# Kernel optimization log

Hardware: AMD Instinct MI355X
Metric: run time of the kernel (lower is better)

The kernel has to match this reference:

```python
import jax, jax.numpy as jnp
import numpy as np

B, S, D = 16, 2048, 128


def setup_inputs() -> dict:
    key = jax.random.key(0)
    k1, k2, k3, k4 = jax.random.split(key, 4)
    return {
        "query": jax.random.normal(k1, (B, S, D), dtype=jnp.float32),
        "key": jax.random.normal(k2, (B, S, D), dtype=jnp.float32),
        "value": jax.random.normal(k3, (B, S, D), dtype=jnp.float32),
        "scale_factor": jax.random.normal(k4, (1, S, S), dtype=jnp.float32),
        "dropout_p": 0,
    }


def reference(query, key, value, scale_factor, dropout_p):
    # qk = Q K^T  -> [B, S, S]
    qk = jnp.einsum("bqd,bkd->bqk", query, key)
    # elementwise scale matrix (broadcast over batch), then row softmax
    scaled_qk = qk * scale_factor
    softmax_qk = jax.nn.softmax(scaled_qk, axis=-1)
    # dropout_p == 0 -> identity (eval-mode / deterministic baseline)
    # output = P V -> [B, S, D]
    return jnp.einsum("bqk,bkd->bqd", softmax_qk, value)
```

## Files before the change

### kernel.cpp

```cpp
#include <hip/hip_runtime.h>
#include <hip/hip_bf16.h>

#define SS 2048
#define DD 128
#define KT 64
#define NT (SS / KT)

typedef float floatx4 __attribute__((ext_vector_type(4)));
typedef __bf16 bf16x8 __attribute__((ext_vector_type(8)));
typedef unsigned short u16x4 __attribute__((ext_vector_type(4)));
typedef unsigned short u16x8 __attribute__((ext_vector_type(8)));

__device__ __forceinline__ int kcol_perm(int d) {
    return ((d >> 5) << 5) | (((d & 15) >> 2) << 3) | (((d >> 4) & 1) << 2) | (d & 3);
}

__device__ __forceinline__ unsigned short bfbits(float x) {
    __bf16 h = (__bf16)x;
    return __builtin_bit_cast(unsigned short, h);
}

__global__ __launch_bounds__(256, 2)
void attn_scaled_kernel(const float* __restrict__ Q, const float* __restrict__ K,
                        const float* __restrict__ V, const float* __restrict__ Sc,
                        float* __restrict__ Out) {
    __shared__ __align__(16) unsigned short Khi[KT * DD];
    __shared__ __align__(16) unsigned short Klo[KT * DD];
    __shared__ __align__(16) unsigned short Vt[DD * KT];

    const int t    = threadIdx.x;
    const int w    = t >> 6;
    const int lane = t & 63;
    const int lq   = lane & 15;
    const int qg   = lane >> 4;

    const int p     = blockIdx.x;
    const int wid   = ((p & 7) << 6) + (p >> 3);
    const int batch = wid >> 5;
    const int q0    = (wid & 31) << 6;

    const float* Qb = Q + (size_t)batch * SS * DD;
    const float* Kb = K + (size_t)batch * SS * DD;
    const float* Vb = V + (size_t)batch * SS * DD;

    const int srow = t >> 5;
    const int c4   = (t & 31) << 2;
    const int kw0  = srow * 128 + (kcol_perm(c4) ^ ((srow & 7) << 3));
    const float* Kp = Kb + (size_t)srow * DD + c4;

    const int vd   = ((w & 1) << 6) + lane;
    const int vkv  = w >> 1;
    const int vswz = (vd & 7) << 3;
    const float* Vp = Vb + vd;

#define STAGE_K(I, KV) do {                                           \
        float ks_[4] = {(KV).x, (KV).y, (KV).z, (KV).w};              \
        u16x4 hh_, ll_;                                               \
        _Pragma("unroll")                                             \
        for (int e_ = 0; e_ < 4; ++e_) {                              \
            __bf16 hb_ = (__bf16)ks_[e_];                             \
            __bf16 lb_ = (__bf16)(ks_[e_] - (float)hb_);              \
            hh_[e_] = __builtin_bit_cast(unsigned short, hb_);        \
            ll_[e_] = __builtin_bit_cast(unsigned short, lb_);        \
        }                                                             \
        *(u16x4*)&Khi[kw0 + 1024 * (I)] = hh_;                        \
        *(u16x4*)&Klo[kw0 + 1024 * (I)] = ll_;                        \
    } while (0)

#define STAGE_V(I, VPI) do {                                          \
        u16x8 vv_;                                                    \
        _Pragma("unroll")                                             \
        for (int e_ = 0; e_ < 8; ++e_) vv_[e_] = bfbits((VPI)[e_]);   \
        *(u16x8*)&Vt[((vd << 6) + (vkv << 5) + ((I) << 3)) ^ vswz] = vv_; \
    } while (0)

#define LOAD_V(I, VPI, BASE) do {                                     \
        _Pragma("unroll")                                             \
        for (int h_ = 0; h_ < 2; ++h_)                                \
            _Pragma("unroll")                                         \
            for (int j_ = 0; j_ < 4; ++j_)                            \
                (VPI)[h_ * 4 + j_] =                                  \
                    Vp[(BASE) + (size_t)((vkv << 5) + ((I) << 2) + (h_ << 4) + j_) * DD]; \
    } while (0)

    const int qrow = q0 + (w << 4) + lq;
    const float* Qr = Qb + (size_t)qrow * DD;
    bf16x8 qh[4], ql[4];
#pragma unroll
    for (int ds = 0; ds < 4; ++ds) {
#pragma unroll
        for (int h = 0; h < 2; ++h) {
            float4 qv = *(const float4*)(Qr + (qg << 2) + (h << 4) + (ds << 5));
            float xs[4] = {qv.x, qv.y, qv.z, qv.w};
#pragma unroll
            for (int e = 0; e < 4; ++e) {
                __bf16 hb = (__bf16)xs[e];
                __bf16 lb = (__bf16)(xs[e] - (float)hb);
                qh[ds][h * 4 + e] = hb;
                ql[ds][h * 4 + e] = lb;
            }
        }
    }

    const float* ScRow = Sc + (size_t)qrow * SS;

    float4 scur0, scur1, scur2, scur3;
    {
        float4 kn[8];
        float  vp[4][8];
#pragma unroll
        for (int i = 0; i < 8; ++i) kn[i] = *(const float4*)(Kp + (size_t)(8 * i) * DD);
#pragma unroll
        for (int i = 0; i < 4; ++i) LOAD_V(i, vp[i], 0);
        scur0 = *(const float4*)(ScRow + 0  + (qg << 2));
        scur1 = *(const float4*)(ScRow + 16 + (qg << 2));
        scur2 = *(const float4*)(ScRow + 32 + (qg << 2));
        scur3 = *(const float4*)(ScRow + 48 + (qg << 2));
#pragma unroll
        for (int i = 0; i < 8; ++i) STAGE_K(i, kn[i]);
#pragma unroll
        for (int i = 0; i < 4; ++i) STAGE_V(i, vp[i]);
    }
    __syncthreads();

    floatx4 O[8];
#pragma unroll
    for (int i = 0; i < 8; ++i) O[i] = (floatx4){0.f, 0.f, 0.f, 0.f};
    float m_run = -INFINITY, l_run = 0.f;

    for (int kt = 0; kt < NT; ++kt) {
        const int kbase = kt << 6;
        const bool pre = (kt + 1 < NT);
        float4 kn[8], scn0, scn1, scn2, scn3;
        float  vp[4][8];
        if (pre) {
            const size_t off = (size_t)(kbase + KT) * DD;
#pragma unroll
            for (int i = 0; i < 8; ++i)
                kn[i] = *(const float4*)(Kp + off + (size_t)(8 * i) * DD);
#pragma unroll
            for (int i = 0; i < 4; ++i) LOAD_V(i, vp[i], off);
            const float* sr = ScRow + kbase + KT;
            scn0 = *(const float4*)(sr + 0  + (qg << 2));
            scn1 = *(const float4*)(sr + 16 + (qg << 2));
            scn2 = *(const float4*)(sr + 32 + (qg << 2));
            scn3 = *(const float4*)(sr + 48 + (qg << 2));
        }

        floatx4 st[4];
#pragma unroll
        for (int g = 0; g < 4; ++g) st[g] = (floatx4){0.f, 0.f, 0.f, 0.f};
        const int sx = (lq & 7) << 3;
        __builtin_amdgcn_s_setprio(1);
#pragma unroll
        for (int ds = 0; ds < 4; ++ds) {
            const int cc = (ds << 5) + (qg << 3);
#pragma unroll
            for (int g = 0; g < 4; ++g) {
                const int b = ((g * 16 + lq) * 128 + cc) ^ sx;
                bf16x8 kh = *(const bf16x8*)&Khi[b];
                bf16x8 kl = *(const bf16x8*)&Klo[b];
                st[g] = __builtin_amdgcn_mfma_f32_16x16x32_bf16(kh, qh[ds], st[g], 0, 0, 0);
                st[g] = __builtin_amdgcn_mfma_f32_16x16x32_bf16(kh, ql[ds], st[g], 0, 0, 0);
                st[g] = __builtin_amdgcn_mfma_f32_16x16x32_bf16(kl, qh[ds], st[g], 0, 0, 0);
            }
        }
        __builtin_amdgcn_s_setprio(0);

        float sv[16];
        sv[0]  = st[0][0] * scur0.x; sv[1]  = st[0][1] * scur0.y;
        sv[2]  = st[0][2] * scur0.z; sv[3]  = st[0][3] * scur0.w;
        sv[4]  = st[1][0] * scur1.x; sv[5]  = st[1][1] * scur1.y;
        sv[6]  = st[1][2] * scur1.z; sv[7]  = st[1][3] * scur1.w;
        sv[8]  = st[2][0] * scur2.x; sv[9]  = st[2][1] * scur2.y;
        sv[10] = st[2][2] * scur2.z; sv[11] = st[2][3] * scur2.w;
        sv[12] = st[3][0] * scur3.x; sv[13] = st[3][1] * scur3.y;
        sv[14] = st[3][2] * scur3.z; sv[15] = st[3][3] * scur3.w;

        float tm = fmaxf(fmaxf(fmaxf(sv[0], sv[1]), fmaxf(sv[2], sv[3])),
                         fmaxf(fmaxf(sv[4], sv[5]), fmaxf(sv[6], sv[7])));
        float tm2 = fmaxf(fmaxf(fmaxf(sv[8], sv[9]), fmaxf(sv[10], sv[11])),
                          fmaxf(fmaxf(sv[12], sv[13]), fmaxf(sv[14], sv[15])));
        tm = fmaxf(tm, tm2);
        tm = fmaxf(tm, __shfl_xor(tm, 16));
        tm = fmaxf(tm, __shfl_xor(tm, 32));
        float mnew  = fmaxf(m_run, tm);
        float alpha = __expf(m_run - mnew);
        m_run = mnew;

        float psum = 0.f;
        bf16x8 pa0, pa1;
#pragma unroll
        for (int e = 0; e < 4; ++e) {
            float p0 = __expf(sv[e]      - mnew);
            float p1 = __expf(sv[4 + e]  - mnew);
            float p2 = __expf(sv[8 + e]  - mnew);
            float p3 = __expf(sv[12 + e] - mnew);
            psum += (p0 + p1) + (p2 + p3);
            pa0[e] = (__bf16)p0; pa0[4 + e] = (__bf16)p1;
            pa1[e] = (__bf16)p2; pa1[4 + e] = (__bf16)p3;
        }
        psum += __shfl_xor(psum, 16);
        psum += __shfl_xor(psum, 32);
        l_run = l_run * alpha + psum;

        float ar0 = __shfl(alpha, (qg << 2) + 0);
        float ar1 = __shfl(alpha, (qg << 2) + 1);
        float ar2 = __shfl(alpha, (qg << 2) + 2);
        float ar3 = __shfl(alpha, (qg << 2) + 3);
#pragma unroll
        for (int df = 0; df < 8; ++df) {
            O[df][0] *= ar0; O[df][1] *= ar1; O[df][2] *= ar2; O[df][3] *= ar3;
        }

        __builtin_amdgcn_s_setprio(1);
#pragma unroll
        for (int df = 0; df < 8; ++df) {
            const int d   = lq + (df << 4);
            const int vb0 = (((d << 6) +      (qg << 3)) ^ sx);
            const int vb1 = (((d << 6) + 32 + (qg << 3)) ^ sx);
            bf16x8 vf0 = *(const bf16x8*)&Vt[vb0];
            bf16x8 vf1 = *(const bf16x8*)&Vt[vb1];
            O[df] = __builtin_amdgcn_mfma_f32_16x16x32_bf16(pa0, vf0, O[df], 0, 0, 0);
            O[df] = __builtin_amdgcn_mfma_f32_16x16x32_bf16(pa1, vf1, O[df], 0, 0, 0);
        }
        __builtin_amdgcn_s_setprio(0);

        if (pre) {
            __syncthreads();
#pragma unroll
            for (int i = 0; i < 8; ++i) STAGE_K(i, kn[i]);
#pragma unroll
            for (int i = 0; i < 4; ++i) STAGE_V(i, vp[i]);
            scur0 = scn0; scur1 = scn1; scur2 = scn2; scur3 = scn3;
            __syncthreads();
        }
    }

    float inv0 = 1.f / __shfl(l_run, (qg << 2) + 0);
    float inv1 = 1.f / __shfl(l_run, (qg << 2) + 1);
    float inv2 = 1.f / __shfl(l_run, (qg << 2) + 2);
    float inv3 = 1.f / __shfl(l_run, (qg << 2) + 3);
    const size_t obase = ((size_t)batch * SS + (size_t)(q0 + (w << 4))) * DD;
#pragma unroll
    for (int df = 0; df < 8; ++df) {
        int d = lq + (df << 4);
        Out[obase + (size_t)((qg << 2) + 0) * DD + d] = O[df][0] * inv0;
        Out[obase + (size_t)((qg << 2) + 1) * DD + d] = O[df][1] * inv1;
        Out[obase + (size_t)((qg << 2) + 2) * DD + d] = O[df][2] * inv2;
        Out[obase + (size_t)((qg << 2) + 3) * DD + d] = O[df][3] * inv3;
    }
#undef STAGE_K
#undef STAGE_V
#undef LOAD_V
}

extern "C" void kernel_launch(void* const* d_in, const int* in_sizes, int n_in,
                              void* d_out, int out_size, void* d_ws, size_t ws_size,
                              hipStream_t stream) {
    const float* q  = (const float*)d_in[0];
    const float* k  = (const float*)d_in[1];
    const float* v  = (const float*)d_in[2];
    const float* sc = (const float*)d_in[3];
    float* out = (float*)d_out;
    hipLaunchKernelGGL(attn_scaled_kernel, dim3(512), dim3(256), 0, stream,
                       q, k, v, sc, out);
}
```

Measured before the change: 230.5 us.

## Process two 16-row query tiles per wave to halve K/V staging

Each wave now owns 32 query rows, as two 16-row sub-tiles, instead of 16. A block covers 128 rows and the grid drops from 512 to 256 blocks, so every K/V tile staged in shared memory feeds twice as many MFMAs. The aim is to halve global K/V reads, bf16 conversion and shared-memory staging per unit of output. In exchange, register use roughly doubles for O, the scores and the Q fragments, launch bounds drop to one block per CU, and there are fewer waves to hide latency.

```diff
diff --git a/kernel.cpp b/kernel.cpp
--- a/kernel.cpp
+++ b/kernel.cpp
@@ -20,7 +20,7 @@
     return __builtin_bit_cast(unsigned short, h);
 }
 
-__global__ __launch_bounds__(256, 2)
+__global__ __launch_bounds__(256, 1)
 void attn_scaled_kernel(const float* __restrict__ Q, const float* __restrict__ K,
                         const float* __restrict__ V, const float* __restrict__ Sc,
                         float* __restrict__ Out) {
@@ -35,9 +35,9 @@
     const int qg   = lane >> 4;
 
     const int p     = blockIdx.x;
-    const int wid   = ((p & 7) << 6) + (p >> 3);
-    const int batch = wid >> 5;
-    const int q0    = (wid & 31) << 6;
+    const int wid   = ((p & 7) << 5) + (p >> 3);
+    const int batch = wid >> 4;
+    const int q0    = (wid & 15) << 7;
 
     const float* Qb = Q + (size_t)batch * SS * DD;
     const float* Kb = K + (size_t)batch * SS * DD;
@@ -83,28 +83,31 @@
                     Vp[(BASE) + (size_t)((vkv << 5) + ((I) << 2) + (h_ << 4) + j_) * DD]; \
     } while (0)
 
-    const int qrow = q0 + (w << 4) + lq;
-    const float* Qr = Qb + (size_t)qrow * DD;
-    bf16x8 qh[4], ql[4];
-#pragma unroll
-    for (int ds = 0; ds < 4; ++ds) {
-#pragma unroll
-        for (int h = 0; h < 2; ++h) {
-            float4 qv = *(const float4*)(Qr + (qg << 2) + (h << 4) + (ds << 5));
-            float xs[4] = {qv.x, qv.y, qv.z, qv.w};
-#pragma unroll
-            for (int e = 0; e < 4; ++e) {
-                __bf16 hb = (__bf16)xs[e];
-                __bf16 lb = (__bf16)(xs[e] - (float)hb);
-                qh[ds][h * 4 + e] = hb;
-                ql[ds][h * 4 + e] = lb;
-            }
-        }
-    }
-
-    const float* ScRow = Sc + (size_t)qrow * SS;
-
-    float4 scur0, scur1, scur2, scur3;
+    const int qrow0 = q0 + (w << 5) + lq;
+    bf16x8 qh[2][4], ql[2][4];
+#pragma unroll
+    for (int h2 = 0; h2 < 2; ++h2) {
+        const float* Qr = Qb + (size_t)(qrow0 + 16 * h2) * DD;
+#pragma unroll
+        for (int ds = 0; ds < 4; ++ds) {
+#pragma unroll
+            for (int h = 0; h < 2; ++h) {
+                float4 qv = *(const float4*)(Qr + (qg << 2) + (h << 4) + (ds << 5));
+                float xs[4] = {qv.x, qv.y, qv.z, qv.w};
+#pragma unroll
+                for (int e = 0; e < 4; ++e) {
+                    __bf16 hb = (__bf16)xs[e];
+                    __bf16 lb = (__bf16)(xs[e] - (float)hb);
+                    qh[h2][ds][h * 4 + e] = hb;
+                    ql[h2][ds][h * 4 + e] = lb;
+                }
+            }
+        }
+    }
+
+    const float* ScRow0 = Sc + (size_t)qrow0 * SS;
+
+    float4 scur[2][4];
     {
         float4 kn[8];
         float  vp[4][8];
@@ -112,10 +115,11 @@
         for (int i = 0; i < 8; ++i) kn[i] = *(const float4*)(Kp + (size_t)(8 * i) * DD);
 #pragma unroll
         for (int i = 0; i < 4; ++i) LOAD_V(i, vp[i], 0);
-        scur0 = *(const float4*)(ScRow + 0  + (qg << 2));
-        scur1 = *(const float4*)(ScRow + 16 + (qg << 2));
-        scur2 = *(const float4*)(ScRow + 32 + (qg << 2));
-        scur3 = *(const float4*)(ScRow + 48 + (qg << 2));
+#pragma unroll
+        for (int h2 = 0; h2 < 2; ++h2)
+#pragma unroll
+            for (int g = 0; g < 4; ++g)
+                scur[h2][g] = *(const float4*)(ScRow0 + (size_t)(h2 * 16) * SS + g * 16 + (qg << 2));
 #pragma unroll
         for (int i = 0; i < 8; ++i) STAGE_K(i, kn[i]);
 #pragma unroll
@@ -123,15 +127,18 @@
     }
     __syncthreads();
 
-    floatx4 O[8];
-#pragma unroll
-    for (int i = 0; i < 8; ++i) O[i] = (floatx4){0.f, 0.f, 0.f, 0.f};
-    float m_run = -INFINITY, l_run = 0.f;
+    floatx4 O[2][8];
+#pragma unroll
+    for (int h2 = 0; h2 < 2; ++h2)
+#pragma unroll
+        for (int i = 0; i < 8; ++i) O[h2][i] = (floatx4){0.f, 0.f, 0.f, 0.f};
+    float m_run[2] = {-INFINITY, -INFINITY};
+    float l_run[2] = {0.f, 0.f};
 
     for (int kt = 0; kt < NT; ++kt) {
         const int kbase = kt << 6;
         const bool pre = (kt + 1 < NT);
-        float4 kn[8], scn0, scn1, scn2, scn3;
+        float4 kn[8], scn[2][4];
         float  vp[4][8];
         if (pre) {
             const size_t off = (size_t)(kbase + KT) * DD;
@@ -140,16 +147,19 @@
                 kn[i] = *(const float4*)(Kp + off + (size_t)(8 * i) * DD);
 #pragma unroll
             for (int i = 0; i < 4; ++i) LOAD_V(i, vp[i], off);
-            const float* sr = ScRow + kbase + KT;
-            scn0 = *(const float4*)(sr + 0  + (qg << 2));
-            scn1 = *(const float4*)(sr + 16 + (qg << 2));
-            scn2 = *(const float4*)(sr + 32 + (qg << 2));
-            scn3 = *(const float4*)(sr + 48 + (qg << 2));
-        }
-
-        floatx4 st[4];
-#pragma unroll
-        for (int g = 0; g < 4; ++g) st[g] = (floatx4){0.f, 0.f, 0.f, 0.f};
+#pragma unroll
+            for (int h2 = 0; h2 < 2; ++h2)
+#pragma unroll
+                for (int g = 0; g < 4; ++g)
+                    scn[h2][g] = *(const float4*)(ScRow0 + (size_t)(h2 * 16) * SS
+                                                  + kbase + KT + g * 16 + (qg << 2));
+        }
+
+        floatx4 st[2][4];
+#pragma unroll
+        for (int h2 = 0; h2 < 2; ++h2)
+#pragma unroll
+            for (int g = 0; g < 4; ++g) st[h2][g] = (floatx4){0.f, 0.f, 0.f, 0.f};
         const int sx = (lq & 7) << 3;
         __builtin_amdgcn_s_setprio(1);
 #pragma unroll
@@ -160,57 +170,62 @@
                 const int b = ((g * 16 + lq) * 128 + cc) ^ sx;
                 bf16x8 kh = *(const bf16x8*)&Khi[b];
                 bf16x8 kl = *(const bf16x8*)&Klo[b];
-                st[g] = __builtin_amdgcn_mfma_f32_16x16x32_bf16(kh, qh[ds], st[g], 0, 0, 0);
-                st[g] = __builtin_amdgcn_mfma_f32_16x16x32_bf16(kh, ql[ds], st[g], 0, 0, 0);
-                st[g] = __builtin_amdgcn_mfma_f32_16x16x32_bf16(kl, qh[ds], st[g], 0, 0, 0);
+#pragma unroll
+                for (int h2 = 0; h2 < 2; ++h2) {
+                    st[h2][g] = __builtin_amdgcn_mfma_f32_16x16x32_bf16(kh, qh[h2][ds], st[h2][g], 0, 0, 0);
+                    st[h2][g] = __builtin_amdgcn_mfma_f32_16x16x32_bf16(kh, ql[h2][ds], st[h2][g], 0, 0, 0);
+                    st[h2][g] = __builtin_amdgcn_mfma_f32_16x16x32_bf16(kl, qh[h2][ds], st[h2][g], 0, 0, 0);
+                }
             }
         }
         __builtin_amdgcn_s_setprio(0);
 
-        float sv[16];
-        sv[0]  = st[0][0] * scur0.x; sv[1]  = st[0][1] * scur0.y;
-        sv[2]  = st[0][2] * scur0.z; sv[3]  = st[0][3] * scur0.w;
-        sv[4]  = st[1][0] * scur1.x; sv[5]  = st[1][1] * scur1.y;
-        sv[6]  = st[1][2] * scur1.z; sv[7]  = st[1][3] * scur1.w;
-        sv[8]  = st[2][0] * scur2.x; sv[9]  = st[2][1] * scur2.y;
-        sv[10] = st[2][2] * scur2.z; sv[11] = st[2][3] * scur2.w;
-        sv[12] = st[3][0] * scur3.x; sv[13] = st[3][1] * scur3.y;
-        sv[14] = st[3][2] * scur3.z; sv[15] = st[3][3] * scur3.w;
-
-        float tm = fmaxf(fmaxf(fmaxf(sv[0], sv[1]), fmaxf(sv[2], sv[3])),
-                         fmaxf(fmaxf(sv[4], sv[5]), fmaxf(sv[6], sv[7])));
-        float tm2 = fmaxf(fmaxf(fmaxf(sv[8], sv[9]), fmaxf(sv[10], sv[11])),
-                          fmaxf(fmaxf(sv[12], sv[13]), fmaxf(sv[14], sv[15])));
-        tm = fmaxf(tm, tm2);
-        tm = fmaxf(tm, __shfl_xor(tm, 16));
-        tm = fmaxf(tm, __shfl_xor(tm, 32));
-        float mnew  = fmaxf(m_run, tm);
-        float alpha = __expf(m_run - mnew);
-        m_run = mnew;
-
-        float psum = 0.f;
-        bf16x8 pa0, pa1;
-#pragma unroll
-        for (int e = 0; e < 4; ++e) {
-            float p0 = __expf(sv[e]      - mnew);
-            float p1 = __expf(sv[4 + e]  - mnew);
-            float p2 = __expf(sv[8 + e]  - mnew);
-            float p3 = __expf(sv[12 + e] - mnew);
-            psum += (p0 + p1) + (p2 + p3);
-            pa0[e] = (__bf16)p0; pa0[4 + e] = (__bf16)p1;
-            pa1[e] = (__bf16)p2; pa1[4 + e] = (__bf16)p3;
-        }
-        psum += __shfl_xor(psum, 16);
-        psum += __shfl_xor(psum, 32);
-        l_run = l_run * alpha + psum;
-
-        float ar0 = __shfl(alpha, (qg << 2) + 0);
-        float ar1 = __shfl(alpha, (qg << 2) + 1);
-        float ar2 = __shfl(alpha, (qg << 2) + 2);
-        float ar3 = __shfl(alpha, (qg << 2) + 3);
-#pragma unroll
-        for (int df = 0; df < 8; ++df) {
-            O[df][0] *= ar0; O[df][1] *= ar1; O[df][2] *= ar2; O[df][3] *= ar3;
+        bf16x8 pa[2][2];
+#pragma unroll
+        for (int h2 = 0; h2 < 2; ++h2) {
+            float sv[16];
+#pragma unroll
+            for (int g = 0; g < 4; ++g) {
+                sv[g * 4 + 0] = st[h2][g][0] * scur[h2][g].x;
+                sv[g * 4 + 1] = st[h2][g][1] * scur[h2][g].y;
+                sv[g * 4 + 2] = st[h2][g][2] * scur[h2][g].z;
+                sv[g * 4 + 3] = st[h2][g][3] * scur[h2][g].w;
+            }
+            float tm = fmaxf(fmaxf(fmaxf(sv[0], sv[1]), fmaxf(sv[2], sv[3])),
+                             fmaxf(fmaxf(sv[4], sv[5]), fmaxf(sv[6], sv[7])));
+            float tm2 = fmaxf(fmaxf(fmaxf(sv[8], sv[9]), fmaxf(sv[10], sv[11])),
+                              fmaxf(fmaxf(sv[12], sv[13]), fmaxf(sv[14], sv[15])));
+            tm = fmaxf(tm, tm2);
+            tm = fmaxf(tm, __shfl_xor(tm, 16));
+            tm = fmaxf(tm, __shfl_xor(tm, 32));
+            float mnew  = fmaxf(m_run[h2], tm);
+            float alpha = __expf(m_run[h2] - mnew);
+            m_run[h2] = mnew;
+
+            float psum = 0.f;
+#pragma unroll
+            for (int e = 0; e < 4; ++e) {
+                float p0 = __expf(sv[e]      - mnew);
+                float p1 = __expf(sv[4 + e]  - mnew);
+                float p2 = __expf(sv[8 + e]  - mnew);
+                float p3 = __expf(sv[12 + e] - mnew);
+                psum += (p0 + p1) + (p2 + p3);
+                pa[h2][0][e] = (__bf16)p0; pa[h2][0][4 + e] = (__bf16)p1;
+                pa[h2][1][e] = (__bf16)p2; pa[h2][1][4 + e] = (__bf16)p3;
+            }
+            psum += __shfl_xor(psum, 16);
+            psum += __shfl_xor(psum, 32);
+            l_run[h2] = l_run[h2] * alpha + psum;
+
+            float ar0 = __shfl(alpha, (qg << 2) + 0);
+            float ar1 = __shfl(alpha, (qg << 2) + 1);
+            float ar2 = __shfl(alpha, (qg << 2) + 2);
+            float ar3 = __shfl(alpha, (qg << 2) + 3);
+#pragma unroll
+            for (int df = 0; df < 8; ++df) {
+                O[h2][df][0] *= ar0; O[h2][df][1] *= ar1;
+                O[h2][df][2] *= ar2; O[h2][df][3] *= ar3;
+            }
         }
 
         __builtin_amdgcn_s_setprio(1);
@@ -221,8 +236,11 @@
             const int vb1 = (((d << 6) + 32 + (qg << 3)) ^ sx);
             bf16x8 vf0 = *(const bf16x8*)&Vt[vb0];
             bf16x8 vf1 = *(const bf16x8*)&Vt[vb1];
-            O[df] = __builtin_amdgcn_mfma_f32_16x16x32_bf16(pa0, vf0, O[df], 0, 0, 0);
-            O[df] = __builtin_amdgcn_mfma_f32_16x16x32_bf16(pa1, vf1, O[df], 0, 0, 0);
+#pragma unroll
+            for (int h2 = 0; h2 < 2; ++h2) {
+                O[h2][df] = __builtin_amdgcn_mfma_f32_16x16x32_bf16(pa[h2][0], vf0, O[h2][df], 0, 0, 0);
+                O[h2][df] = __builtin_amdgcn_mfma_f32_16x16x32_bf16(pa[h2][1], vf1, O[h2][df], 0, 0, 0);
+            }
         }
         __builtin_amdgcn_s_setprio(0);
 
@@ -232,23 +250,29 @@
             for (int i = 0; i < 8; ++i) STAGE_K(i, kn[i]);
 #pragma unroll
             for (int i = 0; i < 4; ++i) STAGE_V(i, vp[i]);
-            scur0 = scn0; scur1 = scn1; scur2 = scn2; scur3 = scn3;
+#pragma unroll
+            for (int h2 = 0; h2 < 2; ++h2)
+#pragma unroll
+                for (int g = 0; g < 4; ++g) scur[h2][g] = scn[h2][g];
             __syncthreads();
         }
     }
 
-    float inv0 = 1.f / __shfl(l_run, (qg << 2) + 0);
-    float inv1 = 1.f / __shfl(l_run, (qg << 2) + 1);
-    float inv2 = 1.f / __shfl(l_run, (qg << 2) + 2);
-    float inv3 = 1.f / __shfl(l_run, (qg << 2) + 3);
-    const size_t obase = ((size_t)batch * SS + (size_t)(q0 + (w << 4))) * DD;
-#pragma unroll
-    for (int df = 0; df < 8; ++df) {
-        int d = lq + (df << 4);
-        Out[obase + (size_t)((qg << 2) + 0) * DD + d] = O[df][0] * inv0;
-        Out[obase + (size_t)((qg << 2) + 1) * DD + d] = O[df][1] * inv1;
-        Out[obase + (size_t)((qg << 2) + 2) * DD + d] = O[df][2] * inv2;
-        Out[obase + (size_t)((qg << 2) + 3) * DD + d] = O[df][3] * inv3;
+#pragma unroll
+    for (int h2 = 0; h2 < 2; ++h2) {
+        float inv0 = 1.f / __shfl(l_run[h2], (qg << 2) + 0);
+        float inv1 = 1.f / __shfl(l_run[h2], (qg << 2) + 1);
+        float inv2 = 1.f / __shfl(l_run[h2], (qg << 2) + 2);
+        float inv3 = 1.f / __shfl(l_run[h2], (qg << 2) + 3);
+        const size_t obase = ((size_t)batch * SS + (size_t)(q0 + (w << 5) + 16 * h2)) * DD;
+#pragma unroll
+        for (int df = 0; df < 8; ++df) {
+            int d = lq + (df << 4);
+            Out[obase + (size_t)((qg << 2) + 0) * DD + d] = O[h2][df][0] * inv0;
+            Out[obase + (size_t)((qg << 2) + 1) * DD + d] = O[h2][df][1] * inv1;
+            Out[obase + (size_t)((qg << 2) + 2) * DD + d] = O[h2][df][2] * inv2;
+            Out[obase + (size_t)((qg << 2) + 3) * DD + d] = O[h2][df][3] * inv3;
+        }
     }
 #undef STAGE_K
 #undef STAGE_V
@@ -263,6 +287,6 @@
     const float* v  = (const float*)d_in[2];
     const float* sc = (const float*)d_in[3];
     float* out = (float*)d_out;
-    hipLaunchKernelGGL(attn_scaled_kernel, dim3(512), dim3(256), 0, stream,
+    hipLaunchKernelGGL(attn_scaled_kernel, dim3(256), dim3(256), 0, stream,
                        q, k, v, sc, out);
 }
```

Result: no change. 227.7 us (-1.2%).
